# Kernel optimization log

Measured on AMD Instinct MI355X. Metric: run time of the kernel, lower is better.

Reference implementation:

```python
import jax, jax.numpy as jnp
import numpy as np

B, S, D, K = 16, 1024, 512, 4
DIL = (1, 2, 4, 8)
EPS_BN = 1e-5
EPS_LN = 1e-5


def _edge_conv1d(x, w, b, dilation):
    # x: [B, C, S], w: [O, C, k]; replicate ('edge') padding keeps length S
    p = (w.shape[-1] - 1) * dilation // 2
    xp = jnp.pad(x, ((0, 0), (0, 0), (p, p)), mode='edge')
    y = jax.lax.conv_general_dilated(xp, w, (1,), 'VALID', rhs_dilation=(dilation,),
                                     dimension_numbers=('NCH', 'OIH', 'NCH'))
    return y + b[None, :, None]


def setup_inputs() -> dict:
    key = jax.random.key(0)
    ks = jax.random.split(key, 16)
    g = lambda i, shape, s: jax.random.normal(ks[i], shape, jnp.float32) * s
    return {
        'x': g(0, (B, S, D), 1.0),
        'conv_w': g(1, (4, D, D, 3), 0.02),
        'conv_b': jnp.zeros((4, D), jnp.float32),
        'fusion_w': g(2, (D, 4 * D), 0.02),
        'fusion_b': jnp.zeros((D,), jnp.float32),
        'refine_w': g(3, (D, D, 3), 0.02),
        'refine_b': jnp.zeros((D,), jnp.float32),
        'hyp1_w': g(4, (D, D, 3), 0.02),
        'hyp1_b': jnp.zeros((D,), jnp.float32),
        'bn_gamma': jnp.ones((D,), jnp.float32),
        'bn_beta': jnp.zeros((D,), jnp.float32),
        'hyp2_w': g(5, (D // 2, D, 3), 0.02),
        'hyp2_b': jnp.zeros((D // 2,), jnp.float32),
        'proj_w': g(6, (2 * K, D // 2), 0.05),
        'proj_b': jnp.zeros((2 * K,), jnp.float32),
        'gate_w': g(7, (D, D), 0.02),
        'gate_b': jnp.zeros((D,), jnp.float32),
        'base_w': g(8, (D, D), 0.02),
        'base_b': jnp.zeros((D,), jnp.float32),
        'wav_w': g(9, (K, D, D), 0.02),
        'wav_b': jnp.zeros((K, D), jnp.float32),
        'ln_gamma': jnp.ones((D,), jnp.float32),
        'ln_beta': jnp.zeros((D,), jnp.float32),
    }


def _forward(x, conv_w, conv_b, fusion_w, fusion_b, refine_w, refine_b,
             hyp1_w, hyp1_b, bn_gamma, bn_beta, hyp2_w, hyp2_b,
             proj_w, proj_b, gate_w, gate_b, base_w, base_b,
             wav_w, wav_b, ln_gamma, ln_beta):
    residual = x
    x_in = jnp.transpose(x, (0, 2, 1))                      # [B, D, S]
    # ---- FFT trend/seasonal split ----
    fx = jnp.fft.rfft(x_in, axis=2)
    cutoff = S // 10
    mask = (jnp.arange(fx.shape[2]) < cutoff).astype(fx.dtype)
    x_seasonal = jnp.fft.irfft(fx * mask, n=S, axis=2)       # [B, D, S]
    x_smooth = x_seasonal
    x_spike = x_in - x_seasonal
    # ---- iterative dilated-conv smoothing (dropout = identity, eval mode) ----
    for _ in range(2):  # iterations
        outs = [jax.nn.gelu(_edge_conv1d(x_smooth, conv_w[i], conv_b[i], DIL[i]),
                            approximate=False)
                for i in range(4)]
        x_concat = jnp.concatenate(outs, axis=1)             # [B, 4D, S]
        x_smooth = jnp.einsum('oc,bcs->bos', fusion_w, x_concat) + fusion_b[None, :, None]
        x_spike = _edge_conv1d(x_in - x_smooth, refine_w, refine_b, 1)
    x_smooth_t = jnp.transpose(x_smooth, (0, 2, 1))          # [B, S, D]
    x_spike_t = jnp.transpose(x_spike, (0, 2, 1))            # [B, S, D]
    # ---- hypernet (BatchNorm in eval mode: running mean 0, var 1) ----
    h = _edge_conv1d(x_smooth, hyp1_w, hyp1_b, 1)
    h = h / jnp.sqrt(1.0 + EPS_BN) * bn_gamma[None, :, None] + bn_beta[None, :, None]
    h = jax.nn.silu(h)
    h = jax.nn.silu(_edge_conv1d(h, hyp2_w, hyp2_b, 1))      # [B, D/2, S]
    cnn_feat = jnp.mean(h, axis=2)                           # AdaptiveAvgPool1d(1)
    params = (cnn_feat @ proj_w.T + proj_b).reshape(B, 1, K, 2)
    dyn_a = jax.nn.softplus(params[..., 0]) + 0.01           # [B, 1, K]
    dyn_b = jax.nn.sigmoid(params[..., 1]) * S               # [B, 1, K]
    # ---- wavelet-KAN base path: Linear(silu(x_smooth)) ----
    base_out = jnp.einsum('bsd,ed->bse', jax.nn.silu(x_smooth_t), base_w) + base_b
    # ---- wavelet path: mexican-hat wavelets over sequence positions ----
    pos = jnp.arange(S, dtype=x.dtype)[None, :, None]        # [1, S, 1]
    u = (pos - dyn_b) / dyn_a                                # [B, S, K]
    c = 2.0 / (np.sqrt(3.0) * np.pi ** 0.25)
    psi = c * (1.0 - u * u) * jnp.exp(-0.5 * u * u)          # [B, S, K]
    z = jnp.einsum('bsd,kde->bkse', x_spike_t, wav_w)        # per-wavelet linear
    kan_out = jnp.einsum('bsk,bkse->bse', psi, z) + jnp.einsum('bsk,ke->bse', psi, wav_b)
    amp = jax.nn.sigmoid(base_out @ gate_w.T + gate_b) * 2.0
    x_out = base_out + kan_out * amp
    # ---- residual + LayerNorm ----
    y = x_out + residual
    mu = jnp.mean(y, axis=-1, keepdims=True)
    var = jnp.var(y, axis=-1, keepdims=True)
    return (y - mu) / jnp.sqrt(var + EPS_LN) * ln_gamma + ln_beta


def reference(x, conv_w, conv_b, fusion_w, fusion_b, refine_w, refine_b,
              hyp1_w, hyp1_b, bn_gamma, bn_beta, hyp2_w, hyp2_b,
              proj_w, proj_b, gate_w, gate_b, base_w, base_b,
              wav_w, wav_b, ln_gamma, ln_beta):
    return _forward(x, conv_w, conv_b, fusion_w, fusion_b, refine_w, refine_b,
                    hyp1_w, hyp1_b, bn_gamma, bn_beta, hyp2_w, hyp2_b,
                    proj_w, proj_b, gate_w, gate_b, base_w, base_b,
                    wav_w, wav_b, ln_gamma, ln_beta)
```

## Files before the change

kernel.cpp:

```cpp
#include <hip/hip_runtime.h>
#include <hip/hip_bf16.h>
#include <math.h>

#define NB 16
#define SS 1024
#define DD 512
#define HD 256

typedef unsigned short US;
typedef short bf16x8 __attribute__((ext_vector_type(8)));
typedef float f32x4 __attribute__((ext_vector_type(4)));
typedef __attribute__((address_space(1))) const void gv1;
typedef __attribute__((address_space(3))) void lv3;

static __device__ __forceinline__ float b2sf(US u){ return __uint_as_float(((unsigned)u)<<16); }
static __device__ __forceinline__ US f2b(float f){
  __hip_bfloat16 h = __float2bfloat16(f);
  union { __hip_bfloat16 h; US u; } c; c.h = h; return c.u;
}
static __device__ __forceinline__ float rd(const void* __restrict__ p, long i, int isf){
  return isf ? ((const float*)p)[i] : b2sf(((const US*)p)[i]);
}

__global__ void k_detect(const void* __restrict__ x, int* __restrict__ flag){
  const US* u = (const US*)x;
  int t = threadIdx.x;
  float m = 0.f;
  for (int i = t; i < 4096; i += 256){
    float v = fabsf(b2sf(u[i]));
    if (isnan(v) || isinf(v)) v = 1e30f;
    m = fmaxf(m, v);
  }
  for (int off = 32; off; off >>= 1) m = fmaxf(m, __shfl_down(m, off));
  __shared__ float sh[4];
  if ((t & 63) == 0) sh[t >> 6] = m;
  __syncthreads();
  if (t == 0){
    float mm = fmaxf(fmaxf(sh[0], sh[1]), fmaxf(sh[2], sh[3]));
    flag[0] = (mm > 1e6f) ? 1 : 0;
  }
}

struct WTab { const void* src[8]; long start[9]; int type[8]; int C[8]; };
__global__ void k_prep_w(WTab wt, US* __restrict__ dst, const int* __restrict__ fl){
  int isf = fl[0];
  long i = (long)blockIdx.x*256 + threadIdx.x;
  if (i >= wt.start[8]) return;
  int s = 0;
  while (i >= wt.start[s+1]) s++;
  long r = i - wt.start[s];
  long si;
  if (wt.type[s] == 0){
    int C = wt.C[s]; long oc3 = 3L*C;
    int o = (int)(r / oc3); int rr = (int)(r - (long)o*oc3); int t = rr / C; int c = rr - t*C;
    si = ((long)o*C + c)*3 + t;
  } else if (wt.type[s] == 1){
    int k = (int)(r >> 18); int e = (int)((r >> 9) & 511); int d = (int)(r & 511);
    si = ((long)(k*512 + d))*512 + e;
  } else si = r;
  dst[i] = f2b(rd(wt.src[s], si, isf));
}

struct FTab { const void* src[14]; int start[15]; };
__global__ void k_cvt_all(FTab ft, float* __restrict__ dst, const int* __restrict__ fl){
  int isf = fl[0];
  int i = blockIdx.x*256 + threadIdx.x;
  if (i >= ft.start[14]) return;
  int s = 0;
  while (i >= ft.start[s+1]) s++;
  dst[i] = rd(ft.src[s], i - ft.start[s], isf);
}

__global__ void k_build_g(float* __restrict__ g){
  int d = blockIdx.x*256 + threadIdx.x;
  if (d >= SS) return;
  float s = 1.f;
  for (int k = 1; k < 102; ++k){
    int r = (k*d) & (SS-1);
    s += 2.f * cosf(6.28318530718f * (float)r * (1.f/SS));
  }
  g[d] = s * (1.f/SS);
}
__global__ void k_build_cmat(const float* __restrict__ g, US* __restrict__ cm){
  int i = blockIdx.x*256 + threadIdx.x;
  if (i >= SS*SS) return;
  int t = i >> 10, s = i & (SS-1);
  cm[i] = f2b(g[(s - t) & (SS-1)]);
}
__global__ __launch_bounds__(256) void k_transpose_b(const void* __restrict__ x, US* __restrict__ xt, const int* __restrict__ fl){
  int isf = fl[0];
  __shared__ float tl[32][33];
  int b = blockIdx.z, s0 = blockIdx.x*32, d0 = blockIdx.y*32;
  int tx = threadIdx.x & 31, ty = threadIdx.x >> 5;
  for (int i = ty; i < 32; i += 8)
    tl[i][tx] = rd(x, ((long)(b*SS + s0+i))*DD + d0+tx, isf);
  __syncthreads();
  for (int i = ty; i < 32; i += 8)
    xt[((long)(b*DD + d0+i))*SS + s0+tx] = f2b(tl[tx][i]);
}
__global__ void k_diff_silu(const US* __restrict__ sm, const void* __restrict__ x,
                            US* __restrict__ diff, US* __restrict__ sils, const int* __restrict__ fl){
  int isf = fl[0];
  long i = (long)blockIdx.x*256 + threadIdx.x;
  if (i >= (long)NB*SS*DD/4) return;
  ushort4 s4 = *(const ushort4*)&sm[i*4];
  float sv[4] = {b2sf(s4.x), b2sf(s4.y), b2sf(s4.z), b2sf(s4.w)};
  float xv[4];
  if (isf){ float4 q = *(const float4*)((const float*)x + i*4); xv[0]=q.x; xv[1]=q.y; xv[2]=q.z; xv[3]=q.w; }
  else { ushort4 q = *(const ushort4*)((const US*)x + i*4); xv[0]=b2sf(q.x); xv[1]=b2sf(q.y); xv[2]=b2sf(q.z); xv[3]=b2sf(q.w); }
  ushort4 d4, l4;
  US* dp = (US*)&d4; US* lp = (US*)&l4;
  #pragma unroll
  for (int r = 0; r < 4; r++){
    dp[r] = f2b(xv[r] - sv[r]);
    lp[r] = f2b(sv[r]/(1.f + expf(-sv[r])));
  }
  *(ushort4*)&diff[i*4] = d4;
  *(ushort4*)&sils[i*4] = l4;
}

template<int EPI, bool TAPPED>
__global__ __launch_bounds__(256) void k_mfma(
    const US* __restrict__ A, const US* __restrict__ Bact, void* __restrict__ Out,
    int NYB, int K, long sBbytes, int ldbB, int dil,
    long sOut, int ldo,
    const float* __restrict__ bias, const float* __restrict__ s1v, const float* __restrict__ s2v,
    const float* __restrict__ psiP)
{
  __shared__ alignas(16) US shb[2*128*64];
  __shared__ float psh[(EPI==4) ? 512 : 4];
  US* As = shb;
  US* Bs = shb + 128*64;
  const int bx = blockIdx.x;
  const int ny = bx % NYB;
  const int b  = bx / NYB;
  const int m0 = blockIdx.y*128, n0 = ny*128;
  const int dd = (TAPPED && dil < 0) ? (1 << (m0 >> 9)) : dil;
  const char* Bb = (const char*)Bact + (long)b*sBbytes;
  const int tid = threadIdx.x;
  const int lane = tid & 63, w = tid >> 6;
  const int wr = w >> 1, wc = w & 1;
  const int col = lane & 15, g = lane >> 4;

  if (EPI == 4){
    for (int i = tid; i < 512; i += 256)
      psh[i] = psiP[(long)b*4096 + (i >> 7)*SS + n0 + (i & 127)];
  }

  f32x4 acc[4][4];
  f32x4 facc[4][4];
  if (EPI == 4){
    #pragma unroll
    for (int i = 0; i < 4; i++)
      #pragma unroll
      for (int j = 0; j < 4; j++) facc[i][j] = (f32x4){0.f,0.f,0.f,0.f};
  }

  int rows_[4], sls_[4];
  #pragma unroll
  for (int i = 0; i < 4; i++){
    int c = w*256 + i*64 + lane;
    rows_[i] = c >> 3;
    sls_[i] = (c & 7) ^ ((c >> 3) & 7);
  }

  const int NKC = (EPI == 4) ? 4 : 1;
  for (int kc = 0; kc < NKC; ++kc){
    #pragma unroll
    for (int i = 0; i < 4; i++)
      #pragma unroll
      for (int j = 0; j < 4; j++) acc[i][j] = (f32x4){0.f,0.f,0.f,0.f};

    for (int k0 = 0; k0 < K; k0 += 64){
      const int c0 = TAPPED ? (k0 & 511) : k0;
      const int tapoff = TAPPED ? (((k0 >> 9) - 1)*dd) : 0;
      __syncthreads();
      #pragma unroll
      for (int i = 0; i < 4; i++){
        const long arow = (long)(m0 + rows_[i]) + (EPI==4 ? kc*512 : 0);
        const char* ga = (const char*)A + (arow*K + k0)*2 + sls_[i]*16;
        __builtin_amdgcn_global_load_lds((gv1*)ga, (lv3*)&As[(w*256 + i*64)*8], 16, 0, 0);
        int brow = n0 + rows_[i] + tapoff;
        if (TAPPED) brow = brow < 0 ? 0 : (brow > SS-1 ? SS-1 : brow);
        const char* gb = Bb + (long)brow*ldbB + c0*2 + sls_[i]*16;
        __builtin_amdgcn_global_load_lds((gv1*)gb, (lv3*)&Bs[(w*256 + i*64)*8], 16, 0, 0);
      }
      __syncthreads();
      #pragma unroll
      for (int kk = 0; kk < 2; kk++){
        bf16x8 af[4], bf[4];
        #pragma unroll
        for (int f = 0; f < 4; f++){
          int rowa = wr*64 + f*16 + col;
          int sla = (g + kk*4) ^ (rowa & 7);
          af[f] = *(const bf16x8*)&As[rowa*64 + sla*8];
          int rowb = wc*64 + f*16 + col;
          int slb = (g + kk*4) ^ (rowb & 7);
          bf[f] = *(const bf16x8*)&Bs[rowb*64 + slb*8];
        }
        #pragma unroll
        for (int fm = 0; fm < 4; fm++)
          #pragma unroll
          for (int fn = 0; fn < 4; fn++)
            acc[fm][fn] = __builtin_amdgcn_mfma_f32_16x16x32_bf16(af[fm], bf[fn], acc[fm][fn], 0, 0, 0);
      }
    }

    if (EPI == 4){
      #pragma unroll
      for (int fm = 0; fm < 4; fm++){
        const int mm_l = wr*64 + fm*16 + g*4;
        float bb[4];
        #pragma unroll
        for (int r = 0; r < 4; r++) bb[r] = bias[kc*512 + m0 + mm_l + r];
        #pragma unroll
        for (int fn = 0; fn < 4; fn++){
          float p = psh[kc*128 + wc*64 + fn*16 + col];
          #pragma unroll
          for (int r = 0; r < 4; r++)
            facc[fm][fn][r] += p * (acc[fm][fn][r] + bb[r]);
        }
      }
    }
  }

  __syncthreads();
  US* tile = shb;
  #pragma unroll
  for (int fm = 0; fm < 4; fm++){
    const int mm_l = wr*64 + fm*16 + g*4;
    float bb[4];
    if (EPI <= 3){
      #pragma unroll
      for (int r = 0; r < 4; r++) bb[r] = bias[m0 + mm_l + r];
    }
    #pragma unroll
    for (int fn = 0; fn < 4; fn++){
      const int nn_l = wc*64 + fn*16 + col;
      f32x4 v = (EPI == 4) ? facc[fm][fn] : acc[fm][fn];
      if (EPI == 5){
        #pragma unroll
        for (int r = 0; r < 4; r++){
          int row = mm_l + r;
          int byte = row*256 + ((nn_l*2) ^ ((row & 7) << 4));
          *(US*)((char*)tile + byte) = f2b(v[r]);
        }
      } else {
        US pk[4];
        #pragma unroll
        for (int r = 0; r < 4; r++){
          float val = v[r];
          if (EPI <= 3) val += bb[r];
          if (EPI == 1) val = 0.5f*val*(1.f + erff(val*0.70710678f));
          if (EPI == 2){ int m = m0 + mm_l + r; val = val*(s1v[m]*0.99999500f) + s2v[m]; val = val/(1.f + expf(-val)); }
          if (EPI == 3){ val = val/(1.f + expf(-val)); }
          pk[r] = f2b(val);
        }
        int byte = nn_l*256 + ((mm_l*2) ^ ((nn_l & 7) << 4));
        *(int2*)((char*)tile + byte) = *(int2*)pk;
      }
    }
  }
  __syncthreads();
  const int r0 = tid >> 4, c = tid & 15;
  #pragma unroll
  for (int p = 0; p < 8; p++){
    int r = p*16 + r0;
    int4 vv = *(const int4*)((const char*)tile + r*256 + ((c*16) ^ ((r & 7) << 4)));
    long obase = (EPI == 5) ? ((long)b*sOut + (long)(m0 + r)*ldo + n0)
                            : ((long)b*sOut + (long)(n0 + r)*ldo + m0);
    *(int4*)((US*)Out + obase + c*8) = vv;
  }
}

__global__ __launch_bounds__(256) void k_pool1(const US* __restrict__ h2, float* __restrict__ part){
  int blk = blockIdx.x;
  int b = blk >> 3, ch = blk & 7;
  int c = threadIdx.x;
  float s = 0.f;
  for (int t = ch*128; t < ch*128 + 128; t++) s += b2sf(h2[((long)(b*SS + t))*HD + c]);
  part[(blk << 8) | c] = s;
}
__global__ __launch_bounds__(256) void k_pool2(const float* __restrict__ part, float* __restrict__ feat){
  int b = blockIdx.x, c = threadIdx.x;
  float s = 0.f;
  for (int ch = 0; ch < 8; ch++) s += part[((b*8 + ch) << 8) | c];
  feat[b*HD + c] = s * (1.f/SS);
}
__global__ void k_params(const float* __restrict__ feat, const float* __restrict__ pw,
                         const float* __restrict__ pb, float* __restrict__ dynA, float* __restrict__ dynB){
  int t = threadIdx.x;
  if (t >= 128) return;
  int b = t >> 3, j = t & 7;
  float s = pb[j];
  for (int c = 0; c < HD; c++) s += feat[b*HD + c]*pw[j*HD + c];
  int k = j >> 1;
  if ((j & 1) == 0){
    float sp = s > 20.f ? s : log1pf(expf(s));
    dynA[b*4 + k] = sp + 0.01f;
  } else {
    dynB[b*4 + k] = 1024.f/(1.f + expf(-s));
  }
}
__global__ void k_psi(const float* __restrict__ dynA, const float* __restrict__ dynB, float* __restrict__ psi){
  int i = blockIdx.x*256 + threadIdx.x;
  if (i >= NB*4*SS) return;
  int b = i >> 12, k = (i >> 10) & 3, s = i & (SS-1);
  float u = ((float)s - dynB[b*4 + k]) / dynA[b*4 + k];
  psi[i] = 0.86732507f*(1.f - u*u)*expf(-0.5f*u*u);
}
__global__ __launch_bounds__(128) void k_final(const US* __restrict__ base, const US* __restrict__ kan,
    const US* __restrict__ gate, const void* __restrict__ x,
    void* __restrict__ out, const float* __restrict__ lng, const float* __restrict__ lnb,
    const int* __restrict__ fl){
  int isf = fl[0];
  long row = blockIdx.x;
  int t = threadIdx.x;
  long off = row*DD + t*4;
  ushort4 bs = *(const ushort4*)&base[off];
  ushort4 gt = *(const ushort4*)&gate[off];
  ushort4 kn = *(const ushort4*)&kan[off];
  float xv[4];
  if (isf){ float4 q = *(const float4*)((const float*)x + off); xv[0]=q.x; xv[1]=q.y; xv[2]=q.z; xv[3]=q.w; }
  else { ushort4 q = *(const ushort4*)((const US*)x + off); xv[0]=b2sf(q.x); xv[1]=b2sf(q.y); xv[2]=b2sf(q.z); xv[3]=b2sf(q.w); }
  float bv[4] = {b2sf(bs.x), b2sf(bs.y), b2sf(bs.z), b2sf(bs.w)};
  float gv[4] = {b2sf(gt.x), b2sf(gt.y), b2sf(gt.z), b2sf(gt.w)};
  const US* kp = (const US*)&kn;
  float y[4];
  float sm = 0.f, ssq = 0.f;
  #pragma unroll
  for (int r = 0; r < 4; r++){
    float amp = 2.f/(1.f + expf(-gv[r]));
    y[r] = bv[r] + b2sf(kp[r])*amp + xv[r];
    sm += y[r]; ssq += y[r]*y[r];
  }
  for (int o = 32; o; o >>= 1){ sm += __shfl_down(sm, o); ssq += __shfl_down(ssq, o); }
  __shared__ float sh[4];
  int lane = t & 63, wid = t >> 6;
  if (lane == 0){ sh[wid*2] = sm; sh[wid*2+1] = ssq; }
  __syncthreads();
  float S1 = sh[0] + sh[2], S2 = sh[1] + sh[3];
  float mean = S1*(1.f/DD), var = S2*(1.f/DD) - mean*mean;
  float rstd = rsqrtf(var + 1e-5f);
  #pragma unroll
  for (int r = 0; r < 4; r++){
    int d = t*4 + r;
    float val = (y[r] - mean)*rstd*lng[d] + lnb[d];
    if (isf) ((float*)out)[off + r] = val;
    else     ((US*)out)[off + r] = f2b(val);
  }
}

extern "C" void kernel_launch(void* const* d_in, const int* in_sizes, int n_in,
                              void* d_out, int out_size, void* d_ws, size_t ws_size,
                              hipStream_t stream){
  const void* x       = d_in[0];
  const void* conv_w  = d_in[1];
  const void* conv_b  = d_in[2];
  const void* fusion_w= d_in[3];
  const void* fusion_b= d_in[4];
  const void* refine_w= d_in[5];
  const void* refine_b= d_in[6];
  const void* hyp1_w  = d_in[7];
  const void* hyp1_b  = d_in[8];
  const void* bn_g    = d_in[9];
  const void* bn_b    = d_in[10];
  const void* hyp2_w  = d_in[11];
  const void* hyp2_b  = d_in[12];
  const void* proj_w  = d_in[13];
  const void* proj_b  = d_in[14];
  const void* gate_w  = d_in[15];
  const void* gate_b  = d_in[16];
  const void* base_w  = d_in[17];
  const void* base_b  = d_in[18];
  const void* wav_w   = d_in[19];
  const void* wav_b   = d_in[20];
  const void* ln_g    = d_in[21];
  const void* ln_b    = d_in[22];

  char* wsb = (char*)d_ws;
  long off = 0;
  auto AA = [&](long bytes)->char*{ char* p = wsb + off; off += (bytes + 255) & ~255L; return p; };
  US* smA   = (US*)AA((long)NB*SS*DD*2);
  US* smB   = (US*)AA((long)NB*SS*DD*2);
  US* xTh   = (US*)AA((long)NB*SS*DD*2);
  US* cc    = (US*)AA((long)NB*SS*2048*2);
  US* baseB = (US*)AA((long)NB*SS*DD*2);
  US* WBLK  = (US*)AA(7733248L*2);
  US* Cm    = (US*)AA(1024L*1024*2);
  float* gvec = (float*)AA(1024*4);
  float* FBLK = (float*)AA(11016L*4);
  float* feat = (float*)AA(16*256*4);
  float* part = (float*)AA(16*8*256*4);
  float* dynA = (float*)AA(64*4);
  float* dynB = (float*)AA(64*4);
  float* psi  = (float*)AA((long)NB*4*SS*4);
  int* flag   = (int*)AA(64);
  if ((size_t)off > ws_size) return;

  US* Wc  = WBLK;
  US* Wr  = Wc  + 3145728L;
  US* Wh1 = Wr  + 786432L;
  US* Wh2 = Wh1 + 786432L;
  US* Wwv = Wh2 + 393216L;
  US* Fw  = Wwv + 1048576L;
  US* BW  = Fw  + 1048576L;
  US* GW  = BW  + 262144L;
  float* cb_f = FBLK;
  float* fz_b = cb_f + 2048;
  float* rf_b = fz_b + 512;
  float* h1_b = rf_b + 512;
  float* h2_b = h1_b + 512;
  float* bs_b = h2_b + 256;
  float* gt_b = bs_b + 512;
  float* wv_b = gt_b + 512;
  float* bngf = wv_b + 2048;
  float* bnbf = bngf + 512;
  float* pwf  = bnbf + 512;
  float* pbf  = pwf  + 2048;
  float* lngf = pbf  + 8;
  float* lnbf = lngf + 512;
  US* diff  = cc;
  US* h2b   = cc;
  US* kanb  = cc + 8388608L;
  US* siluS = cc + 16777216L;

  auto g1 = [](long n){ return dim3((unsigned)((n + 255)/256)); };
  const long sAct = (long)SS*DD*2;
  const long sCC  = (long)SS*2048*2;
  const long oAct = (long)SS*DD;
  const long oCC  = (long)SS*2048;
  const long oH2  = (long)SS*HD;

  k_detect<<<1, 256, 0, stream>>>(x, flag);

  {
    WTab wt;
    const void* srcs[8] = {conv_w, refine_w, hyp1_w, hyp2_w, wav_w, fusion_w, base_w, gate_w};
    long sizes[8] = {3145728, 786432, 786432, 393216, 1048576, 1048576, 262144, 262144};
    int types[8] = {0,0,0,0,1,2,2,2};
    int Cs[8]    = {512,512,512,512,0,0,0,0};
    long acc_ = 0;
    for (int i = 0; i < 8; i++){ wt.src[i]=srcs[i]; wt.start[i]=acc_; wt.type[i]=types[i]; wt.C[i]=Cs[i]; acc_ += sizes[i]; }
    wt.start[8] = acc_;
    k_prep_w<<<g1(acc_), 256, 0, stream>>>(wt, WBLK, flag);
  }
  {
    FTab ft;
    const void* srcs[14] = {conv_b, fusion_b, refine_b, hyp1_b, hyp2_b, base_b, gate_b,
                            wav_b, bn_g, bn_b, proj_w, proj_b, ln_g, ln_b};
    int sizes[14] = {2048,512,512,512,256,512,512,2048,512,512,2048,8,512,512};
    int acc_ = 0;
    for (int i = 0; i < 14; i++){ ft.src[i]=srcs[i]; ft.start[i]=acc_; acc_ += sizes[i]; }
    ft.start[14] = acc_;
    k_cvt_all<<<g1(acc_), 256, 0, stream>>>(ft, FBLK, flag);
  }
  k_build_g<<<g1(SS), 256, 0, stream>>>(gvec);
  k_build_cmat<<<g1((long)SS*SS), 256, 0, stream>>>(gvec, Cm);
  k_transpose_b<<<dim3(SS/32, DD/32, NB), 256, 0, stream>>>(x, xTh, flag);

  k_mfma<5,false><<<dim3(4*NB, 8), 256, 0, stream>>>(Cm, xTh, smA,
      4, 1024, (long)DD*SS*2, SS*2, 0, oAct, DD, nullptr, nullptr, nullptr, nullptr);

  US* cur = smA; US* nxt = smB;
  for (int it = 0; it < 2; ++it){
    k_mfma<1,true><<<dim3(8*NB, 16), 256, 0, stream>>>(Wc, cur, cc,
        8, 1536, sAct, DD*2, -1, oCC, 2048, cb_f, nullptr, nullptr, nullptr);
    k_mfma<0,false><<<dim3(8*NB, 4), 256, 0, stream>>>(Fw, cc, nxt,
        8, 2048, sCC, 4096, 0, oAct, DD, fz_b, nullptr, nullptr, nullptr);
    US* t = cur; cur = nxt; nxt = t;
  }

  k_diff_silu<<<g1((long)NB*SS*DD/4), 256, 0, stream>>>(cur, x, diff, siluS, flag);

  k_mfma<0,true><<<dim3(8*NB, 4), 256, 0, stream>>>(Wr, diff, smB,
      8, 1536, sAct, DD*2, 1, oAct, DD, rf_b, nullptr, nullptr, nullptr);

  k_mfma<2,true><<<dim3(8*NB, 4), 256, 0, stream>>>(Wh1, cur, xTh,
      8, 1536, sAct, DD*2, 1, oAct, DD, h1_b, bngf, bnbf, nullptr);
  k_mfma<3,true><<<dim3(8*NB, 2), 256, 0, stream>>>(Wh2, xTh, h2b,
      8, 1536, sAct, DD*2, 1, oH2, HD, h2_b, nullptr, nullptr, nullptr);
  k_pool1<<<NB*8, 256, 0, stream>>>(h2b, part);
  k_pool2<<<NB, 256, 0, stream>>>(part, feat);
  k_params<<<1, 128, 0, stream>>>(feat, pwf, pbf, dynA, dynB);
  k_psi<<<g1(NB*4*SS), 256, 0, stream>>>(dynA, dynB, psi);

  k_mfma<0,false><<<dim3(8*NB, 4), 256, 0, stream>>>(BW, siluS, baseB,
      8, 512, sAct, DD*2, 0, oAct, DD, bs_b, nullptr, nullptr, nullptr);
  k_mfma<0,false><<<dim3(8*NB, 4), 256, 0, stream>>>(GW, baseB, xTh,
      8, 512, sAct, DD*2, 0, oAct, DD, gt_b, nullptr, nullptr, nullptr);

  k_mfma<4,false><<<dim3(8*NB, 4), 256, 0, stream>>>(Wwv, smB, kanb,
      8, 512, sAct, DD*2, 0, oAct, DD, wv_b, nullptr, nullptr, psi);

  k_final<<<NB*SS, 128, 0, stream>>>(baseB, kanb, xTh, x, d_out, lngf, lnbf, flag);
}
```

Measured before the change: 680.4 us.

## Add 256x256 pipelined MFMA kernel for dilated convs, fuse diff/silu into fusion epilogue

```diff
diff --git a/kernel.cpp b/kernel.cpp
--- a/kernel.cpp
+++ b/kernel.cpp
@@ -98,25 +98,147 @@
   for (int i = ty; i < 32; i += 8)
     xt[((long)(b*DD + d0+i))*SS + s0+tx] = f2b(tl[tx][i]);
 }
-__global__ void k_diff_silu(const US* __restrict__ sm, const void* __restrict__ x,
-                            US* __restrict__ diff, US* __restrict__ sils, const int* __restrict__ fl){
-  int isf = fl[0];
-  long i = (long)blockIdx.x*256 + threadIdx.x;
-  if (i >= (long)NB*SS*DD/4) return;
-  ushort4 s4 = *(const ushort4*)&sm[i*4];
-  float sv[4] = {b2sf(s4.x), b2sf(s4.y), b2sf(s4.z), b2sf(s4.w)};
-  float xv[4];
-  if (isf){ float4 q = *(const float4*)((const float*)x + i*4); xv[0]=q.x; xv[1]=q.y; xv[2]=q.z; xv[3]=q.w; }
-  else { ushort4 q = *(const ushort4*)((const US*)x + i*4); xv[0]=b2sf(q.x); xv[1]=b2sf(q.y); xv[2]=b2sf(q.z); xv[3]=b2sf(q.w); }
-  ushort4 d4, l4;
-  US* dp = (US*)&d4; US* lp = (US*)&l4;
-  #pragma unroll
-  for (int r = 0; r < 4; r++){
-    dp[r] = f2b(xv[r] - sv[r]);
-    lp[r] = f2b(sv[r]/(1.f + expf(-sv[r])));
-  }
-  *(ushort4*)&diff[i*4] = d4;
-  *(ushort4*)&sils[i*4] = l4;
+
+template<int EPI, bool TAPPED>
+__global__ __launch_bounds__(512, 2) void k_mfma8(
+    const US* __restrict__ A, const US* __restrict__ Bact, void* __restrict__ Out,
+    int NYB, int K, long sBbytes, int ldbB, int dil,
+    long sOut, int ldo, const float* __restrict__ bias)
+{
+  __shared__ US ring[65536];
+  const int bx = blockIdx.x;
+  const int ny = bx % NYB, b = bx / NYB;
+  const int m0 = blockIdx.y*256, n0 = ny*256;
+  const int dd = (TAPPED && dil < 0) ? (1 << (m0 >> 9)) : dil;
+  const char* Bb = (const char*)Bact + (long)b*sBbytes;
+  const int tid = threadIdx.x;
+  const int lane = tid & 63, w = tid >> 6;
+  const int wm = w >> 2, wn = w & 3;
+  const int col = lane & 15, g = lane >> 4;
+  const int NTs = K >> 5;
+
+  int offA[8], offB[4];
+  #pragma unroll
+  for (int fm = 0; fm < 8; fm++){
+    int r = wm*128 + fm*16 + col;
+    int R = r >> 1;
+    int wg = ((r & 1) << 2) | g;
+    offA[fm] = R*128 + ((wg ^ (R & 7)) << 4);
+  }
+  #pragma unroll
+  for (int fn = 0; fn < 4; fn++){
+    int r = wn*64 + fn*16 + col;
+    int R = r >> 1;
+    int wg = ((r & 1) << 2) | g;
+    offB[fn] = R*128 + ((wg ^ (R & 7)) << 4);
+  }
+  int rl[2], gg[2];
+  #pragma unroll
+  for (int j = 0; j < 2; j++){
+    int c = (w*2 + j)*64 + lane;
+    int R = c >> 3, f = c & 7;
+    int wg = f ^ (R & 7);
+    rl[j] = 2*R + (wg >> 2);
+    gg[j] = wg & 3;
+  }
+
+  auto stageA = [&](int t){
+    int slot = t & 3, kb = t << 5;
+    #pragma unroll
+    for (int j = 0; j < 2; j++){
+      const char* ga = (const char*)A + ((long)(m0 + rl[j])*K + kb + gg[j]*8)*2;
+      __builtin_amdgcn_global_load_lds((gv1*)ga, (lv3*)&ring[slot*8192 + (w*2 + j)*512], 16, 0, 0);
+    }
+  };
+  auto stageB = [&](int t){
+    int slot = t & 3, kb = t << 5;
+    int c0 = TAPPED ? (kb & 511) : kb;
+    int tapoff = TAPPED ? (((kb >> 9) - 1)*dd) : 0;
+    #pragma unroll
+    for (int j = 0; j < 2; j++){
+      int brow = n0 + rl[j] + tapoff;
+      if (TAPPED) brow = brow < 0 ? 0 : (brow > SS-1 ? SS-1 : brow);
+      const char* gb = Bb + (long)brow*ldbB + (c0 + gg[j]*8)*2;
+      __builtin_amdgcn_global_load_lds((gv1*)gb, (lv3*)&ring[32768 + slot*8192 + (w*2 + j)*512], 16, 0, 0);
+    }
+  };
+
+  f32x4 acc[8][4];
+  #pragma unroll
+  for (int i = 0; i < 8; i++)
+    #pragma unroll
+    for (int j = 0; j < 4; j++) acc[i][j] = (f32x4){0.f,0.f,0.f,0.f};
+
+  stageA(0); stageB(0);
+  if (NTs > 1){ stageA(1); stageB(1); }
+  if (NTs > 2) stageA(2);
+  asm volatile("s_waitcnt vmcnt(6)" ::: "memory");
+  __builtin_amdgcn_s_barrier();
+
+  bf16x8 af[4], bf[4];
+  for (int ks = 0; ks < NTs; ++ks){
+    const char* As = (const char*)&ring[(ks & 3)*8192];
+    const char* Bs = (const char*)&ring[32768 + (ks & 3)*8192];
+    #pragma unroll
+    for (int fn = 0; fn < 4; fn++) bf[fn] = *(const bf16x8*)(Bs + offB[fn]);
+    #pragma unroll
+    for (int fm = 0; fm < 4; fm++) af[fm] = *(const bf16x8*)(As + offA[fm]);
+    if (ks + 2 < NTs) stageB(ks + 2);
+    __builtin_amdgcn_s_barrier();
+    __builtin_amdgcn_s_setprio(1);
+    #pragma unroll
+    for (int fm = 0; fm < 4; fm++)
+      #pragma unroll
+      for (int fn = 0; fn < 4; fn++)
+        acc[fm][fn] = __builtin_amdgcn_mfma_f32_16x16x32_bf16(af[fm], bf[fn], acc[fm][fn], 0, 0, 0);
+    __builtin_amdgcn_s_setprio(0);
+    __builtin_amdgcn_s_barrier();
+    #pragma unroll
+    for (int fm = 0; fm < 4; fm++) af[fm] = *(const bf16x8*)(As + offA[4 + fm]);
+    if (ks + 3 < NTs) stageA(ks + 3);
+    __builtin_amdgcn_s_barrier();
+    __builtin_amdgcn_s_setprio(1);
+    #pragma unroll
+    for (int fm = 0; fm < 4; fm++)
+      #pragma unroll
+      for (int fn = 0; fn < 4; fn++)
+        acc[4 + fm][fn] = __builtin_amdgcn_mfma_f32_16x16x32_bf16(af[fm], bf[fn], acc[4 + fm][fn], 0, 0, 0);
+    __builtin_amdgcn_s_setprio(0);
+    if (ks < NTs - 3)       asm volatile("s_waitcnt vmcnt(6)" ::: "memory");
+    else if (ks == NTs - 3) asm volatile("s_waitcnt vmcnt(4)" ::: "memory");
+    else if (ks == NTs - 2) asm volatile("s_waitcnt vmcnt(0)" ::: "memory");
+    __builtin_amdgcn_s_barrier();
+  }
+
+  US* tile = ring;
+  #pragma unroll
+  for (int fm = 0; fm < 8; fm++){
+    int m_l = wm*128 + fm*16 + g*4;
+    float4 bb = *(const float4*)&bias[m0 + m_l];
+    const float* bp = (const float*)&bb;
+    #pragma unroll
+    for (int fn = 0; fn < 4; fn++){
+      int n_l = wn*64 + fn*16 + col;
+      f32x4 v = acc[fm][fn];
+      US pk[4];
+      #pragma unroll
+      for (int r = 0; r < 4; r++){
+        float val = v[r] + bp[r];
+        if (EPI == 1) val = 0.5f*val*(1.f + erff(val*0.70710678f));
+        pk[r] = f2b(val);
+      }
+      long byte = (long)n_l*512 + ((((m_l >> 3) ^ (n_l & 7)) << 4) | ((m_l & 7)*2));
+      *(int2*)((char*)tile + byte) = *(int2*)pk;
+    }
+  }
+  __syncthreads();
+  #pragma unroll
+  for (int p = 0; p < 16; p++){
+    int chunk = p*512 + tid;
+    int rr = chunk >> 5, cg = chunk & 31;
+    int4 vv = *(const int4*)((const char*)tile + (long)rr*512 + ((cg ^ (rr & 7)) << 4));
+    *(int4*)((US*)Out + (long)b*sOut + (long)(n0 + rr)*ldo + m0 + cg*8) = vv;
+  }
 }
 
 template<int EPI, bool TAPPED>
@@ -125,7 +247,8 @@
     int NYB, int K, long sBbytes, int ldbB, int dil,
     long sOut, int ldo,
     const float* __restrict__ bias, const float* __restrict__ s1v, const float* __restrict__ s2v,
-    const float* __restrict__ psiP)
+    const float* __restrict__ psiP, const void* __restrict__ xres,
+    US* __restrict__ aux1, US* __restrict__ aux2, const int* __restrict__ fl)
 {
   __shared__ alignas(16) US shb[2*128*64];
   __shared__ float psh[(EPI==4) ? 512 : 4];
@@ -134,8 +257,8 @@
   const int bx = blockIdx.x;
   const int ny = bx % NYB;
   const int b  = bx / NYB;
-  const int m0 = blockIdx.y*128, n0 = ny*128;
-  const int dd = (TAPPED && dil < 0) ? (1 << (m0 >> 9)) : dil;
+  const int m00 = blockIdx.y*128, n0 = ny*128;
+  const int dd = (TAPPED && dil < 0) ? (1 << (m00 >> 9)) : dil;
   const char* Bb = (const char*)Bact + (long)b*sBbytes;
   const int tid = threadIdx.x;
   const int lane = tid & 63, w = tid >> 6;
@@ -177,7 +300,7 @@
       __syncthreads();
       #pragma unroll
       for (int i = 0; i < 4; i++){
-        const long arow = (long)(m0 + rows_[i]) + (EPI==4 ? kc*512 : 0);
+        const long arow = (long)(m00 + rows_[i]) + (EPI==4 ? kc*512 : 0);
         const char* ga = (const char*)A + (arow*K + k0)*2 + sls_[i]*16;
         __builtin_amdgcn_global_load_lds((gv1*)ga, (lv3*)&As[(w*256 + i*64)*8], 16, 0, 0);
         int brow = n0 + rows_[i] + tapoff;
@@ -212,7 +335,7 @@
         const int mm_l = wr*64 + fm*16 + g*4;
         float bb[4];
         #pragma unroll
-        for (int r = 0; r < 4; r++) bb[r] = bias[kc*512 + m0 + mm_l + r];
+        for (int r = 0; r < 4; r++) bb[r] = bias[kc*512 + m00 + mm_l + r];
         #pragma unroll
         for (int fn = 0; fn < 4; fn++){
           float p = psh[kc*128 + wc*64 + fn*16 + col];
@@ -230,9 +353,9 @@
   for (int fm = 0; fm < 4; fm++){
     const int mm_l = wr*64 + fm*16 + g*4;
     float bb[4];
-    if (EPI <= 3){
-      #pragma unroll
-      for (int r = 0; r < 4; r++) bb[r] = bias[m0 + mm_l + r];
+    if (EPI == 0 || EPI == 2 || EPI == 3 || EPI == 6){
+      #pragma unroll
+      for (int r = 0; r < 4; r++) bb[r] = bias[m00 + mm_l + r];
     }
     #pragma unroll
     for (int fn = 0; fn < 4; fn++){
@@ -250,9 +373,8 @@
         #pragma unroll
         for (int r = 0; r < 4; r++){
           float val = v[r];
-          if (EPI <= 3) val += bb[r];
-          if (EPI == 1) val = 0.5f*val*(1.f + erff(val*0.70710678f));
-          if (EPI == 2){ int m = m0 + mm_l + r; val = val*(s1v[m]*0.99999500f) + s2v[m]; val = val/(1.f + expf(-val)); }
+          if (EPI != 4) val += bb[r];
+          if (EPI == 2){ int m = m00 + mm_l + r; val = val*(s1v[m]*0.99999500f) + s2v[m]; val = val/(1.f + expf(-val)); }
           if (EPI == 3){ val = val/(1.f + expf(-val)); }
           pk[r] = f2b(val);
         }
@@ -263,13 +385,28 @@
   }
   __syncthreads();
   const int r0 = tid >> 4, c = tid & 15;
+  const int isf = (EPI == 6) ? fl[0] : 0;
   #pragma unroll
   for (int p = 0; p < 8; p++){
     int r = p*16 + r0;
     int4 vv = *(const int4*)((const char*)tile + r*256 + ((c*16) ^ ((r & 7) << 4)));
-    long obase = (EPI == 5) ? ((long)b*sOut + (long)(m0 + r)*ldo + n0)
-                            : ((long)b*sOut + (long)(n0 + r)*ldo + m0);
+    long obase = (EPI == 5) ? ((long)b*sOut + (long)(m00 + r)*ldo + n0)
+                            : ((long)b*sOut + (long)(n0 + r)*ldo + m00);
     *(int4*)((US*)Out + obase + c*8) = vv;
+    if (EPI == 6){
+      long eb = obase + c*8;
+      const US* vp = (const US*)&vv;
+      US dpk[8], lpk[8];
+      #pragma unroll
+      for (int q = 0; q < 8; q++){
+        float sv = b2sf(vp[q]);
+        float xv = rd(xres, eb + q, isf);
+        dpk[q] = f2b(xv - sv);
+        lpk[q] = f2b(sv/(1.f + expf(-sv)));
+      }
+      *(int4*)&aux1[eb] = *(int4*)dpk;
+      *(int4*)&aux2[eb] = *(int4*)lpk;
+    }
   }
 }
 
@@ -420,10 +557,10 @@
   float* pbf  = pwf  + 2048;
   float* lngf = pbf  + 8;
   float* lnbf = lngf + 512;
-  US* diff  = cc;
-  US* h2b   = cc;
-  US* kanb  = cc + 8388608L;
-  US* siluS = cc + 16777216L;
+  US* spike = cc;
+  US* baseO = cc + 8388608L;
+  US* kanb  = cc + 16777216L;
+  US* h2b   = cc + 25165824L;
 
   auto g1 = [](long n){ return dim3((unsigned)((n + 255)/256)); };
   const long sAct = (long)SS*DD*2;
@@ -434,8 +571,7 @@
 
   k_detect<<<1, 256, 0, stream>>>(x, flag);
 
-  {
-    WTab wt;
+  { WTab wt;
     const void* srcs[8] = {conv_w, refine_w, hyp1_w, hyp2_w, wav_w, fusion_w, base_w, gate_w};
     long sizes[8] = {3145728, 786432, 786432, 393216, 1048576, 1048576, 262144, 262144};
     int types[8] = {0,0,0,0,1,2,2,2};
@@ -445,8 +581,7 @@
     wt.start[8] = acc_;
     k_prep_w<<<g1(acc_), 256, 0, stream>>>(wt, WBLK, flag);
   }
-  {
-    FTab ft;
+  { FTab ft;
     const void* srcs[14] = {conv_b, fusion_b, refine_b, hyp1_b, hyp2_b, base_b, gate_b,
                             wav_b, bn_g, bn_b, proj_w, proj_b, ln_g, ln_b};
     int sizes[14] = {2048,512,512,512,256,512,512,2048,512,512,2048,8,512,512};
@@ -460,38 +595,45 @@
   k_transpose_b<<<dim3(SS/32, DD/32, NB), 256, 0, stream>>>(x, xTh, flag);
 
   k_mfma<5,false><<<dim3(4*NB, 8), 256, 0, stream>>>(Cm, xTh, smA,
-      4, 1024, (long)DD*SS*2, SS*2, 0, oAct, DD, nullptr, nullptr, nullptr, nullptr);
-
-  US* cur = smA; US* nxt = smB;
-  for (int it = 0; it < 2; ++it){
-    k_mfma<1,true><<<dim3(8*NB, 16), 256, 0, stream>>>(Wc, cur, cc,
-        8, 1536, sAct, DD*2, -1, oCC, 2048, cb_f, nullptr, nullptr, nullptr);
-    k_mfma<0,false><<<dim3(8*NB, 4), 256, 0, stream>>>(Fw, cc, nxt,
-        8, 2048, sCC, 4096, 0, oAct, DD, fz_b, nullptr, nullptr, nullptr);
-    US* t = cur; cur = nxt; nxt = t;
-  }
-
-  k_diff_silu<<<g1((long)NB*SS*DD/4), 256, 0, stream>>>(cur, x, diff, siluS, flag);
-
-  k_mfma<0,true><<<dim3(8*NB, 4), 256, 0, stream>>>(Wr, diff, smB,
-      8, 1536, sAct, DD*2, 1, oAct, DD, rf_b, nullptr, nullptr, nullptr);
-
-  k_mfma<2,true><<<dim3(8*NB, 4), 256, 0, stream>>>(Wh1, cur, xTh,
-      8, 1536, sAct, DD*2, 1, oAct, DD, h1_b, bngf, bnbf, nullptr);
+      4, 1024, (long)DD*SS*2, SS*2, 0, oAct, DD,
+      nullptr, nullptr, nullptr, nullptr, nullptr, nullptr, nullptr, nullptr);
+
+  k_mfma8<1,true><<<dim3(4*NB, 8), 512, 0, stream>>>(Wc, smA, cc,
+      4, 1536, sAct, DD*2, -1, oCC, 2048, cb_f);
+  k_mfma<0,false><<<dim3(8*NB, 4), 256, 0, stream>>>(Fw, cc, smB,
+      8, 2048, sCC, 4096, 0, oAct, DD,
+      fz_b, nullptr, nullptr, nullptr, nullptr, nullptr, nullptr, nullptr);
+  k_mfma8<1,true><<<dim3(4*NB, 8), 512, 0, stream>>>(Wc, smB, cc,
+      4, 1536, sAct, DD*2, -1, oCC, 2048, cb_f);
+  k_mfma<6,false><<<dim3(8*NB, 4), 256, 0, stream>>>(Fw, cc, smA,
+      8, 2048, sCC, 4096, 0, oAct, DD,
+      fz_b, nullptr, nullptr, nullptr, x, smB, baseB, flag);
+
+  k_mfma<0,true><<<dim3(8*NB, 4), 256, 0, stream>>>(Wr, smB, spike,
+      8, 1536, sAct, DD*2, 1, oAct, DD,
+      rf_b, nullptr, nullptr, nullptr, nullptr, nullptr, nullptr, nullptr);
+
+  k_mfma<2,true><<<dim3(8*NB, 4), 256, 0, stream>>>(Wh1, smA, xTh,
+      8, 1536, sAct, DD*2, 1, oAct, DD,
+      h1_b, bngf, bnbf, nullptr, nullptr, nullptr, nullptr, nullptr);
   k_mfma<3,true><<<dim3(8*NB, 2), 256, 0, stream>>>(Wh2, xTh, h2b,
-      8, 1536, sAct, DD*2, 1, oH2, HD, h2_b, nullptr, nullptr, nullptr);
+      8, 1536, sAct, DD*2, 1, oH2, HD,
+      h2_b, nullptr, nullptr, nullptr, nullptr, nullptr, nullptr, nullptr);
   k_pool1<<<NB*8, 256, 0, stream>>>(h2b, part);
   k_pool2<<<NB, 256, 0, stream>>>(part, feat);
   k_params<<<1, 128, 0, stream>>>(feat, pwf, pbf, dynA, dynB);
   k_psi<<<g1(NB*4*SS), 256, 0, stream>>>(dynA, dynB, psi);
 
-  k_mfma<0,false><<<dim3(8*NB, 4), 256, 0, stream>>>(BW, siluS, baseB,
-      8, 512, sAct, DD*2, 0, oAct, DD, bs_b, nullptr, nullptr, nullptr);
-  k_mfma<0,false><<<dim3(8*NB, 4), 256, 0, stream>>>(GW, baseB, xTh,
-      8, 512, sAct, DD*2, 0, oAct, DD, gt_b, nullptr, nullptr, nullptr);
-
-  k_mfma<4,false><<<dim3(8*NB, 4), 256, 0, stream>>>(Wwv, smB, kanb,
-      8, 512, sAct, DD*2, 0, oAct, DD, wv_b, nullptr, nullptr, psi);
-
-  k_final<<<NB*SS, 128, 0, stream>>>(baseB, kanb, xTh, x, d_out, lngf, lnbf, flag);
-}
+  k_mfma<0,false><<<dim3(8*NB, 4), 256, 0, stream>>>(BW, baseB, baseO,
+      8, 512, sAct, DD*2, 0, oAct, DD,
+      bs_b, nullptr, nullptr, nullptr, nullptr, nullptr, nullptr, nullptr);
+  k_mfma<0,false><<<dim3(8*NB, 4), 256, 0, stream>>>(GW, baseO, xTh,
+      8, 512, sAct, DD*2, 0, oAct, DD,
+      gt_b, nullptr, nullptr, nullptr, nullptr, nullptr, nullptr, nullptr);
+
+  k_mfma<4,false><<<dim3(8*NB, 4), 256, 0, stream>>>(Wwv, spike, kanb,
+      8, 512, sAct, DD*2, 0, oAct, DD,
+      wv_b, nullptr, nullptr, psi, nullptr, nullptr, nullptr, nullptr);
+
+  k_final<<<NB*SS, 128, 0, stream>>>(baseO, kanb, xTh, x, d_out, lngf, lnbf, flag);
+}
```

After: 671.2 us. No clear change (-1.4%).

## Factor low-pass circulant into rank-203 DFT basis and fuse diff/SiLU epilogue

Applied to the files above, without the earlier changes.

```diff
diff --git a/kernel.cpp b/kernel.cpp
--- a/kernel.cpp
+++ b/kernel.cpp
@@ -71,22 +71,24 @@
   dst[i] = rd(ft.src[s], i - ft.start[s], isf);
 }
 
-__global__ void k_build_g(float* __restrict__ g){
-  int d = blockIdx.x*256 + threadIdx.x;
-  if (d >= SS) return;
-  float s = 1.f;
-  for (int k = 1; k < 102; ++k){
-    int r = (k*d) & (SS-1);
-    s += 2.f * cosf(6.28318530718f * (float)r * (1.f/SS));
-  }
-  g[d] = s * (1.f/SS);
-}
-__global__ void k_build_cmat(const float* __restrict__ g, US* __restrict__ cm){
+__global__ void k_build_p(US* __restrict__ P, US* __restrict__ Pt){
   int i = blockIdx.x*256 + threadIdx.x;
-  if (i >= SS*SS) return;
-  int t = i >> 10, s = i & (SS-1);
-  cm[i] = f2b(g[(s - t) & (SS-1)]);
-}
+  if (i >= 262144) return;
+  int r = i & 255, t = i >> 8;
+  float v;
+  if (r == 0) v = 0.03125f;
+  else if (r <= 101){
+    int ph = (r*t) & 1023;
+    v = 0.04419417382f * cosf(6.28318530718f * (float)ph * (1.f/1024.f));
+  } else if (r <= 202){
+    int ph = ((r-101)*t) & 1023;
+    v = 0.04419417382f * sinf(6.28318530718f * (float)ph * (1.f/1024.f));
+  } else v = 0.f;
+  US b = f2b(v);
+  P[t*256 + r] = b;
+  Pt[r*1024 + t] = b;
+}
+
 __global__ __launch_bounds__(256) void k_transpose_b(const void* __restrict__ x, US* __restrict__ xt, const int* __restrict__ fl){
   int isf = fl[0];
   __shared__ float tl[32][33];
@@ -98,26 +100,6 @@
   for (int i = ty; i < 32; i += 8)
     xt[((long)(b*DD + d0+i))*SS + s0+tx] = f2b(tl[tx][i]);
 }
-__global__ void k_diff_silu(const US* __restrict__ sm, const void* __restrict__ x,
-                            US* __restrict__ diff, US* __restrict__ sils, const int* __restrict__ fl){
-  int isf = fl[0];
-  long i = (long)blockIdx.x*256 + threadIdx.x;
-  if (i >= (long)NB*SS*DD/4) return;
-  ushort4 s4 = *(const ushort4*)&sm[i*4];
-  float sv[4] = {b2sf(s4.x), b2sf(s4.y), b2sf(s4.z), b2sf(s4.w)};
-  float xv[4];
-  if (isf){ float4 q = *(const float4*)((const float*)x + i*4); xv[0]=q.x; xv[1]=q.y; xv[2]=q.z; xv[3]=q.w; }
-  else { ushort4 q = *(const ushort4*)((const US*)x + i*4); xv[0]=b2sf(q.x); xv[1]=b2sf(q.y); xv[2]=b2sf(q.z); xv[3]=b2sf(q.w); }
-  ushort4 d4, l4;
-  US* dp = (US*)&d4; US* lp = (US*)&l4;
-  #pragma unroll
-  for (int r = 0; r < 4; r++){
-    dp[r] = f2b(xv[r] - sv[r]);
-    lp[r] = f2b(sv[r]/(1.f + expf(-sv[r])));
-  }
-  *(ushort4*)&diff[i*4] = d4;
-  *(ushort4*)&sils[i*4] = l4;
-}
 
 template<int EPI, bool TAPPED>
 __global__ __launch_bounds__(256) void k_mfma(
@@ -125,7 +107,8 @@
     int NYB, int K, long sBbytes, int ldbB, int dil,
     long sOut, int ldo,
     const float* __restrict__ bias, const float* __restrict__ s1v, const float* __restrict__ s2v,
-    const float* __restrict__ psiP)
+    const float* __restrict__ psiP, const void* __restrict__ xres,
+    US* __restrict__ aux1, US* __restrict__ aux2, const int* __restrict__ fl)
 {
   __shared__ alignas(16) US shb[2*128*64];
   __shared__ float psh[(EPI==4) ? 512 : 4];
@@ -134,8 +117,8 @@
   const int bx = blockIdx.x;
   const int ny = bx % NYB;
   const int b  = bx / NYB;
-  const int m0 = blockIdx.y*128, n0 = ny*128;
-  const int dd = (TAPPED && dil < 0) ? (1 << (m0 >> 9)) : dil;
+  const int m00 = blockIdx.y*128, n0 = ny*128;
+  const int dd = (TAPPED && dil < 0) ? (1 << (m00 >> 9)) : dil;
   const char* Bb = (const char*)Bact + (long)b*sBbytes;
   const int tid = threadIdx.x;
   const int lane = tid & 63, w = tid >> 6;
@@ -177,7 +160,7 @@
       __syncthreads();
       #pragma unroll
       for (int i = 0; i < 4; i++){
-        const long arow = (long)(m0 + rows_[i]) + (EPI==4 ? kc*512 : 0);
+        const long arow = (long)(m00 + rows_[i]) + (EPI==4 ? kc*512 : 0);
         const char* ga = (const char*)A + (arow*K + k0)*2 + sls_[i]*16;
         __builtin_amdgcn_global_load_lds((gv1*)ga, (lv3*)&As[(w*256 + i*64)*8], 16, 0, 0);
         int brow = n0 + rows_[i] + tapoff;
@@ -212,7 +195,7 @@
         const int mm_l = wr*64 + fm*16 + g*4;
         float bb[4];
         #pragma unroll
-        for (int r = 0; r < 4; r++) bb[r] = bias[kc*512 + m0 + mm_l + r];
+        for (int r = 0; r < 4; r++) bb[r] = bias[kc*512 + m00 + mm_l + r];
         #pragma unroll
         for (int fn = 0; fn < 4; fn++){
           float p = psh[kc*128 + wc*64 + fn*16 + col];
@@ -230,9 +213,9 @@
   for (int fm = 0; fm < 4; fm++){
     const int mm_l = wr*64 + fm*16 + g*4;
     float bb[4];
-    if (EPI <= 3){
-      #pragma unroll
-      for (int r = 0; r < 4; r++) bb[r] = bias[m0 + mm_l + r];
+    if (EPI == 0 || EPI == 1 || EPI == 2 || EPI == 3 || EPI == 6){
+      #pragma unroll
+      for (int r = 0; r < 4; r++) bb[r] = bias[m00 + mm_l + r];
     }
     #pragma unroll
     for (int fn = 0; fn < 4; fn++){
@@ -250,9 +233,9 @@
         #pragma unroll
         for (int r = 0; r < 4; r++){
           float val = v[r];
-          if (EPI <= 3) val += bb[r];
+          if (EPI != 4) val += bb[r];
           if (EPI == 1) val = 0.5f*val*(1.f + erff(val*0.70710678f));
-          if (EPI == 2){ int m = m0 + mm_l + r; val = val*(s1v[m]*0.99999500f) + s2v[m]; val = val/(1.f + expf(-val)); }
+          if (EPI == 2){ int m = m00 + mm_l + r; val = val*(s1v[m]*0.99999500f) + s2v[m]; val = val/(1.f + expf(-val)); }
           if (EPI == 3){ val = val/(1.f + expf(-val)); }
           pk[r] = f2b(val);
         }
@@ -263,13 +246,28 @@
   }
   __syncthreads();
   const int r0 = tid >> 4, c = tid & 15;
+  const int isf = (EPI == 6) ? fl[0] : 0;
   #pragma unroll
   for (int p = 0; p < 8; p++){
     int r = p*16 + r0;
     int4 vv = *(const int4*)((const char*)tile + r*256 + ((c*16) ^ ((r & 7) << 4)));
-    long obase = (EPI == 5) ? ((long)b*sOut + (long)(m0 + r)*ldo + n0)
-                            : ((long)b*sOut + (long)(n0 + r)*ldo + m0);
+    long obase = (EPI == 5) ? ((long)b*sOut + (long)(m00 + r)*ldo + n0)
+                            : ((long)b*sOut + (long)(n0 + r)*ldo + m00);
     *(int4*)((US*)Out + obase + c*8) = vv;
+    if (EPI == 6){
+      long eb = obase + c*8;
+      const US* vp = (const US*)&vv;
+      US dpk[8], lpk[8];
+      #pragma unroll
+      for (int q = 0; q < 8; q++){
+        float sv = b2sf(vp[q]);
+        float xv = rd(xres, eb + q, isf);
+        dpk[q] = f2b(xv - sv);
+        lpk[q] = f2b(sv/(1.f + expf(-sv)));
+      }
+      *(int4*)&aux1[eb] = *(int4*)dpk;
+      *(int4*)&aux2[eb] = *(int4*)lpk;
+    }
   }
 }
 
@@ -287,27 +285,28 @@
   for (int ch = 0; ch < 8; ch++) s += part[((b*8 + ch) << 8) | c];
   feat[b*HD + c] = s * (1.f/SS);
 }
-__global__ void k_params(const float* __restrict__ feat, const float* __restrict__ pw,
-                         const float* __restrict__ pb, float* __restrict__ dynA, float* __restrict__ dynB){
+__global__ __launch_bounds__(1024) void k_hyper(const float* __restrict__ feat, const float* __restrict__ pw,
+    const float* __restrict__ pb, float* __restrict__ psi){
+  __shared__ float dA[64], dB[64];
   int t = threadIdx.x;
-  if (t >= 128) return;
-  int b = t >> 3, j = t & 7;
-  float s = pb[j];
-  for (int c = 0; c < HD; c++) s += feat[b*HD + c]*pw[j*HD + c];
-  int k = j >> 1;
-  if ((j & 1) == 0){
-    float sp = s > 20.f ? s : log1pf(expf(s));
-    dynA[b*4 + k] = sp + 0.01f;
-  } else {
-    dynB[b*4 + k] = 1024.f/(1.f + expf(-s));
-  }
-}
-__global__ void k_psi(const float* __restrict__ dynA, const float* __restrict__ dynB, float* __restrict__ psi){
-  int i = blockIdx.x*256 + threadIdx.x;
-  if (i >= NB*4*SS) return;
-  int b = i >> 12, k = (i >> 10) & 3, s = i & (SS-1);
-  float u = ((float)s - dynB[b*4 + k]) / dynA[b*4 + k];
-  psi[i] = 0.86732507f*(1.f - u*u)*expf(-0.5f*u*u);
+  if (t < 128){
+    int b = t >> 3, j = t & 7;
+    float s = pb[j];
+    for (int c = 0; c < HD; c++) s += feat[b*HD + c]*pw[j*HD + c];
+    int k = j >> 1;
+    if ((j & 1) == 0){
+      float sp = s > 20.f ? s : log1pf(expf(s));
+      dA[b*4 + k] = sp + 0.01f;
+    } else {
+      dB[b*4 + k] = 1024.f/(1.f + expf(-s));
+    }
+  }
+  __syncthreads();
+  for (int i = t; i < NB*4*SS; i += 1024){
+    int b = i >> 12, k = (i >> 10) & 3, s = i & (SS-1);
+    float u = ((float)s - dB[b*4 + k]) / dA[b*4 + k];
+    psi[i] = 0.86732507f*(1.f - u*u)*expf(-0.5f*u*u);
+  }
 }
 __global__ __launch_bounds__(128) void k_final(const US* __restrict__ base, const US* __restrict__ kan,
     const US* __restrict__ gate, const void* __restrict__ x,
@@ -387,13 +386,11 @@
   US* cc    = (US*)AA((long)NB*SS*2048*2);
   US* baseB = (US*)AA((long)NB*SS*DD*2);
   US* WBLK  = (US*)AA(7733248L*2);
-  US* Cm    = (US*)AA(1024L*1024*2);
-  float* gvec = (float*)AA(1024*4);
-  float* FBLK = (float*)AA(11016L*4);
+  US* Pm    = (US*)AA(1024L*256*2);
+  US* Ptm   = (US*)AA(256L*1024*2);
+  float* FBLK = (float*)AA((11016L + 256)*4);
   float* feat = (float*)AA(16*256*4);
   float* part = (float*)AA(16*8*256*4);
-  float* dynA = (float*)AA(64*4);
-  float* dynB = (float*)AA(64*4);
   float* psi  = (float*)AA((long)NB*4*SS*4);
   int* flag   = (int*)AA(64);
   if ((size_t)off > ws_size) return;
@@ -420,10 +417,12 @@
   float* pbf  = pwf  + 2048;
   float* lngf = pbf  + 8;
   float* lnbf = lngf + 512;
-  US* diff  = cc;
-  US* h2b   = cc;
-  US* kanb  = cc + 8388608L;
-  US* siluS = cc + 16777216L;
+  float* zb   = lnbf + 512;
+  US* tmpb  = cc;
+  US* spike = cc;
+  US* baseO = cc + 8388608L;
+  US* kanb  = cc + 16777216L;
+  US* h2b   = cc + 25165824L;
 
   auto g1 = [](long n){ return dim3((unsigned)((n + 255)/256)); };
   const long sAct = (long)SS*DD*2;
@@ -434,8 +433,7 @@
 
   k_detect<<<1, 256, 0, stream>>>(x, flag);
 
-  {
-    WTab wt;
+  { WTab wt;
     const void* srcs[8] = {conv_w, refine_w, hyp1_w, hyp2_w, wav_w, fusion_w, base_w, gate_w};
     long sizes[8] = {3145728, 786432, 786432, 393216, 1048576, 1048576, 262144, 262144};
     int types[8] = {0,0,0,0,1,2,2,2};
@@ -445,8 +443,7 @@
     wt.start[8] = acc_;
     k_prep_w<<<g1(acc_), 256, 0, stream>>>(wt, WBLK, flag);
   }
-  {
-    FTab ft;
+  { FTab ft;
     const void* srcs[14] = {conv_b, fusion_b, refine_b, hyp1_b, hyp2_b, base_b, gate_b,
                             wav_b, bn_g, bn_b, proj_w, proj_b, ln_g, ln_b};
     int sizes[14] = {2048,512,512,512,256,512,512,2048,512,512,2048,8,512,512};
@@ -455,43 +452,54 @@
     ft.start[14] = acc_;
     k_cvt_all<<<g1(acc_), 256, 0, stream>>>(ft, FBLK, flag);
   }
-  k_build_g<<<g1(SS), 256, 0, stream>>>(gvec);
-  k_build_cmat<<<g1((long)SS*SS), 256, 0, stream>>>(gvec, Cm);
+  hipMemsetAsync(zb, 0, 256*sizeof(float), stream);
+  k_build_p<<<g1(262144), 256, 0, stream>>>(Pm, Ptm);
   k_transpose_b<<<dim3(SS/32, DD/32, NB), 256, 0, stream>>>(x, xTh, flag);
 
-  k_mfma<5,false><<<dim3(4*NB, 8), 256, 0, stream>>>(Cm, xTh, smA,
-      4, 1024, (long)DD*SS*2, SS*2, 0, oAct, DD, nullptr, nullptr, nullptr, nullptr);
-
-  US* cur = smA; US* nxt = smB;
-  for (int it = 0; it < 2; ++it){
-    k_mfma<1,true><<<dim3(8*NB, 16), 256, 0, stream>>>(Wc, cur, cc,
-        8, 1536, sAct, DD*2, -1, oCC, 2048, cb_f, nullptr, nullptr, nullptr);
-    k_mfma<0,false><<<dim3(8*NB, 4), 256, 0, stream>>>(Fw, cc, nxt,
-        8, 2048, sCC, 4096, 0, oAct, DD, fz_b, nullptr, nullptr, nullptr);
-    US* t = cur; cur = nxt; nxt = t;
-  }
-
-  k_diff_silu<<<g1((long)NB*SS*DD/4), 256, 0, stream>>>(cur, x, diff, siluS, flag);
-
-  k_mfma<0,true><<<dim3(8*NB, 4), 256, 0, stream>>>(Wr, diff, smB,
-      8, 1536, sAct, DD*2, 1, oAct, DD, rf_b, nullptr, nullptr, nullptr);
-
-  k_mfma<2,true><<<dim3(8*NB, 4), 256, 0, stream>>>(Wh1, cur, xTh,
-      8, 1536, sAct, DD*2, 1, oAct, DD, h1_b, bngf, bnbf, nullptr);
+  k_mfma<0,false><<<dim3(4*NB, 2), 256, 0, stream>>>(Ptm, xTh, tmpb,
+      4, 1024, (long)DD*SS*2, SS*2, 0, (long)DD*256, 256,
+      zb, nullptr, nullptr, nullptr, nullptr, nullptr, nullptr, nullptr);
+  k_mfma<5,false><<<dim3(4*NB, 8), 256, 0, stream>>>(Pm, tmpb, smA,
+      4, 256, (long)DD*256*2, 256*2, 0, oAct, DD,
+      nullptr, nullptr, nullptr, nullptr, nullptr, nullptr, nullptr, nullptr);
+
+  k_mfma<1,true><<<dim3(8*NB, 16), 256, 0, stream>>>(Wc, smA, cc,
+      8, 1536, sAct, DD*2, -1, oCC, 2048,
+      cb_f, nullptr, nullptr, nullptr, nullptr, nullptr, nullptr, nullptr);
+  k_mfma<0,false><<<dim3(8*NB, 4), 256, 0, stream>>>(Fw, cc, smB,
+      8, 2048, sCC, 4096, 0, oAct, DD,
+      fz_b, nullptr, nullptr, nullptr, nullptr, nullptr, nullptr, nullptr);
+  k_mfma<1,true><<<dim3(8*NB, 16), 256, 0, stream>>>(Wc, smB, cc,
+      8, 1536, sAct, DD*2, -1, oCC, 2048,
+      cb_f, nullptr, nullptr, nullptr, nullptr, nullptr, nullptr, nullptr);
+  k_mfma<6,false><<<dim3(8*NB, 4), 256, 0, stream>>>(Fw, cc, smA,
+      8, 2048, sCC, 4096, 0, oAct, DD,
+      fz_b, nullptr, nullptr, nullptr, x, smB, baseB, flag);
+
+  k_mfma<0,true><<<dim3(8*NB, 4), 256, 0, stream>>>(Wr, smB, spike,
+      8, 1536, sAct, DD*2, 1, oAct, DD,
+      rf_b, nullptr, nullptr, nullptr, nullptr, nullptr, nullptr, nullptr);
+
+  k_mfma<2,true><<<dim3(8*NB, 4), 256, 0, stream>>>(Wh1, smA, xTh,
+      8, 1536, sAct, DD*2, 1, oAct, DD,
+      h1_b, bngf, bnbf, nullptr, nullptr, nullptr, nullptr, nullptr);
   k_mfma<3,true><<<dim3(8*NB, 2), 256, 0, stream>>>(Wh2, xTh, h2b,
-      8, 1536, sAct, DD*2, 1, oH2, HD, h2_b, nullptr, nullptr, nullptr);
+      8, 1536, sAct, DD*2, 1, oH2, HD,
+      h2_b, nullptr, nullptr, nullptr, nullptr, nullptr, nullptr, nullptr);
   k_pool1<<<NB*8, 256, 0, stream>>>(h2b, part);
   k_pool2<<<NB, 256, 0, stream>>>(part, feat);
-  k_params<<<1, 128, 0, stream>>>(feat, pwf, pbf, dynA, dynB);
-  k_psi<<<g1(NB*4*SS), 256, 0, stream>>>(dynA, dynB, psi);
-
-  k_mfma<0,false><<<dim3(8*NB, 4), 256, 0, stream>>>(BW, siluS, baseB,
-      8, 512, sAct, DD*2, 0, oAct, DD, bs_b, nullptr, nullptr, nullptr);
-  k_mfma<0,false><<<dim3(8*NB, 4), 256, 0, stream>>>(GW, baseB, xTh,
-      8, 512, sAct, DD*2, 0, oAct, DD, gt_b, nullptr, nullptr, nullptr);
-
-  k_mfma<4,false><<<dim3(8*NB, 4), 256, 0, stream>>>(Wwv, smB, kanb,
-      8, 512, sAct, DD*2, 0, oAct, DD, wv_b, nullptr, nullptr, psi);
-
-  k_final<<<NB*SS, 128, 0, stream>>>(baseB, kanb, xTh, x, d_out, lngf, lnbf, flag);
-}
+  k_hyper<<<1, 1024, 0, stream>>>(feat, pwf, pbf, psi);
+
+  k_mfma<0,false><<<dim3(8*NB, 4), 256, 0, stream>>>(BW, baseB, baseO,
+      8, 512, sAct, DD*2, 0, oAct, DD,
+      bs_b, nullptr, nullptr, nullptr, nullptr, nullptr, nullptr, nullptr);
+  k_mfma<0,false><<<dim3(8*NB, 4), 256, 0, stream>>>(GW, baseO, xTh,
+      8, 512, sAct, DD*2, 0, oAct, DD,
+      gt_b, nullptr, nullptr, nullptr, nullptr, nullptr, nullptr, nullptr);
+
+  k_mfma<4,false><<<dim3(8*NB, 4), 256, 0, stream>>>(Wwv, spike, kanb,
+      8, 512, sAct, DD*2, 0, oAct, DD,
+      wv_b, nullptr, nullptr, psi, nullptr, nullptr, nullptr, nullptr);
+
+  k_final<<<NB*SS, 128, 0, stream>>>(baseO, kanb, xTh, x, d_out, lngf, lnbf, flag);
+}
```

After: 687.7 us. Within noise of the previous version (+1.1%).
